# Performance work log

Measured on AMD Instinct MI355X. Metric: run time of the kernel, lower is better.

The kernel has to match this reference:

```python
import jax, jax.numpy as jnp
import numpy as np

N, E, F_IN, F_OUT, PERIODS = 40000, 640000, 64, 128, 12


def setup_inputs() -> dict:
    key = jax.random.key(0)
    ks = jax.random.split(key, 24)
    def w(k, shape):
        return jax.random.normal(k, shape, jnp.float32) * 0.05
    inp = {
        "X": jax.random.normal(ks[0], (N, F_IN, PERIODS), jnp.float32),
        "edge_index": jax.random.randint(ks[1], (2, E), 0, N),
        "edge_weight": jax.random.uniform(ks[2], (E,), jnp.float32),
        "attention": jax.random.uniform(ks[3], (PERIODS,), jnp.float32),
    }
    for idx, g in enumerate(["i", "f", "c", "o"]):
        inp[f"W_x{g}"] = w(ks[4 + 4 * idx], (F_IN, F_OUT))
        inp[f"b_x{g}"] = jnp.zeros((F_OUT,), jnp.float32)
        inp[f"W_h{g}"] = w(ks[5 + 4 * idx], (2 * F_OUT, F_OUT))
        inp[f"b_h{g}"] = jnp.zeros((F_OUT,), jnp.float32)
    return inp


def reference(X, edge_index, edge_weight, attention,
              W_xi, b_xi, W_hi, b_hi,
              W_xf, b_xf, W_hf, b_hf,
              W_xc, b_xc, W_hc, b_hc,
              W_xo, b_xo, W_ho, b_ho):
    n = X.shape[0]
    # GCN normalization with self-loops: D^-1/2 (A + I) D^-1/2
    loops = jnp.arange(n)
    rows = jnp.concatenate([edge_index[0], loops])  # sources
    cols = jnp.concatenate([edge_index[1], loops])  # targets
    wts = jnp.concatenate([edge_weight, jnp.ones((n,), X.dtype)])
    deg = jax.ops.segment_sum(wts, cols, num_segments=n)
    dinv = jnp.where(deg > 0, jax.lax.rsqrt(deg), 0.0)
    norm = dinv[rows] * wts * dinv[cols]  # [E+N]

    def gcn(x, W, b):
        xw = x @ W  # [N, F_OUT]
        agg = jax.ops.segment_sum(norm[:, None] * xw[rows], cols, num_segments=n)
        return agg + b

    probs = jax.nn.softmax(attention)
    H0 = jnp.zeros((n, W_hi.shape[1]), X.dtype)
    C0 = jnp.zeros_like(H0)
    Xp = jnp.moveaxis(X, 2, 0)  # [periods, N, F_IN]

    def step(carry, xs):
        H, C, Hacc = carry
        x_t, p = xs
        def gate(Wx, bx, Wh, bh):
            return jnp.concatenate([gcn(x_t, Wx, bx), H], axis=1) @ Wh + bh
        I = jax.nn.sigmoid(gate(W_xi, b_xi, W_hi, b_hi))
        F = jax.nn.sigmoid(gate(W_xf, b_xf, W_hf, b_hf))
        Ct = jnp.tanh(gate(W_xc, b_xc, W_hc, b_hc))
        O = jax.nn.sigmoid(gate(W_xo, b_xo, W_ho, b_ho))
        C_new = F * C + I * Ct
        H_new = O * jnp.tanh(C_new)
        return (H_new, C_new, Hacc + p * H_new), None

    (H, C, Hacc), _ = jax.lax.scan(step, (H0, C0, H0), (Xp, probs))
    return Hacc
```

## Files before the change

### kernel.cpp

```cpp
#include <hip/hip_runtime.h>

typedef __bf16 bf16_t;
typedef bf16_t bf16x4 __attribute__((ext_vector_type(4)));
typedef bf16_t bf16x8 __attribute__((ext_vector_type(8)));
typedef float floatx4 __attribute__((ext_vector_type(4)));

#define F_INq 64
#define F_OUTq 128
#define PERIODSq 12
#define XROW (F_INq * PERIODSq)

__global__ __launch_bounds__(256) void k_init(float* deg, int* counts, int N) {
  int i = blockIdx.x * 256 + threadIdx.x;
  if (i < N) { deg[i] = 1.0f; counts[i] = 0; }
}

__global__ __launch_bounds__(256) void k_accum(const int* __restrict__ ei, const float* __restrict__ ew,
                                               float* deg, int* counts, int E) {
  int e = blockIdx.x * 256 + threadIdx.x;
  if (e < E) {
    int c = ei[E + e];
    atomicAdd(&deg[c], ew[e]);
    atomicAdd(&counts[c], 1);
  }
}

__global__ __launch_bounds__(256) void k_dinv(float* deg, int N) {
  int i = blockIdx.x * 256 + threadIdx.x;
  if (i < N) { float d = deg[i]; deg[i] = d > 0.0f ? rsqrtf(d) : 0.0f; }
}

__global__ __launch_bounds__(256) void k_scanA(const int* __restrict__ counts, float* __restrict__ deg,
                                               int* __restrict__ bsum, int N) {
  __shared__ int ws[4];
  int b = blockIdx.x, t = threadIdx.x;
  int base = b * 1024 + t * 4;
  int s = 0;
  if (base + 3 < N) {
    int4 c = *(const int4*)(counts + base);
    s = c.x + c.y + c.z + c.w;
  } else {
    for (int k = 0; k < 4; ++k) if (base + k < N) s += counts[base + k];
  }
#pragma unroll
  for (int k = 0; k < 4; ++k) {
    int idx = base + k;
    if (idx < N) { deg[idx] = rsqrtf(deg[idx] + 1.0f); }
  }
  for (int off = 1; off < 64; off <<= 1) s += __shfl_xor(s, off);
  int lane = t & 63, w = t >> 6;
  if (lane == 0) ws[w] = s;
  __syncthreads();
  if (t == 0) bsum[b] = ws[0] + ws[1] + ws[2] + ws[3];
}

__global__ __launch_bounds__(256) void k_scanC(const int* __restrict__ counts, const int* __restrict__ bsum,
                                               int* __restrict__ offs, int* __restrict__ cursor, int N, int nb) {
  __shared__ int ws[4];
  int b = blockIdx.x, t = threadIdx.x;
  int base = b * 1024 + t * 4;
  int c0_ = 0, c1_ = 0, c2_ = 0, c3_ = 0;
  if (base + 3 < N) {
    int4 c = *(const int4*)(counts + base);
    c0_ = c.x; c1_ = c.y; c2_ = c.z; c3_ = c.w;
  } else {
    if (base < N) c0_ = counts[base];
    if (base + 1 < N) c1_ = counts[base + 1];
    if (base + 2 < N) c2_ = counts[base + 2];
    if (base + 3 < N) c3_ = counts[base + 3];
  }
  int tot = c0_ + c1_ + c2_ + c3_;
  int lane = t & 63, w = t >> 6;
  int inc = tot;
  for (int off = 1; off < 64; off <<= 1) {
    int u = __shfl_up(inc, off);
    if (lane >= off) inc += u;
  }
  if (lane == 63) ws[w] = inc;
  __syncthreads();
  int wb = 0;
  for (int i = 0; i < b; ++i) wb += bsum[i];
  for (int i = 0; i < w; ++i) wb += ws[i];
  int e = wb + inc - tot;
  if (base < N)     { offs[base] = e;                 cursor[base] = e; }
  if (base + 1 < N) { int o = e + c0_;                offs[base + 1] = o; cursor[base + 1] = o; }
  if (base + 2 < N) { int o = e + c0_ + c1_;          offs[base + 2] = o; cursor[base + 2] = o; }
  if (base + 3 < N) { int o = e + c0_ + c1_ + c2_;    offs[base + 3] = o; cursor[base + 3] = o; }
  if (b == nb - 1 && t == 0) {
    int tt2 = 0;
    for (int i = 0; i < nb - 1; ++i) tt2 += bsum[i];
    offs[N] = tt2 + ws[0] + ws[1] + ws[2] + ws[3];
  }
}

__global__ __launch_bounds__(1024) void k_scan(const int* __restrict__ counts, int* __restrict__ offs,
                                               int* __restrict__ cursor, int N) {
  __shared__ int sd[1024];
  int t = threadIdx.x;
  int CH = (N + 1023) >> 10;
  int base = t * CH;
  int sum = 0;
  for (int i = 0; i < CH; ++i) { int idx = base + i; if (idx < N) sum += counts[idx]; }
  sd[t] = sum;
  __syncthreads();
  for (int off = 1; off < 1024; off <<= 1) {
    int v = (t >= off) ? sd[t - off] : 0;
    __syncthreads();
    sd[t] += v;
    __syncthreads();
  }
  int run = sd[t] - sum;
  for (int i = 0; i < CH; ++i) {
    int idx = base + i;
    if (idx < N) { offs[idx] = run; cursor[idx] = run; run += counts[idx]; }
  }
  if (t == 1023) offs[N] = sd[1023];
}

__global__ __launch_bounds__(256) void k_scatter(const int* __restrict__ ei, const float* __restrict__ ew,
                                                 const float* __restrict__ dinv, int* cursor,
                                                 int* __restrict__ csr_src, float* __restrict__ csr_nrm, int E) {
  int e = blockIdx.x * 256 + threadIdx.x;
  if (e < E) {
    int r = ei[e], c = ei[E + e];
    int p = atomicAdd(&cursor[c], 1);
    csr_src[p] = r;
    csr_nrm[p] = dinv[r] * ew[e] * dinv[c];
  }
}

__global__ __launch_bounds__(256) void k_prew(
    const float* __restrict__ Wxi, const float* __restrict__ Whi,
    const float* __restrict__ Wxf, const float* __restrict__ Whf,
    const float* __restrict__ Wxc, const float* __restrict__ Whc,
    const float* __restrict__ Wxo, const float* __restrict__ Who,
    const float* __restrict__ bxi, const float* __restrict__ bhi,
    const float* __restrict__ bxf, const float* __restrict__ bhf,
    const float* __restrict__ bxc, const float* __restrict__ bhc,
    const float* __restrict__ bxo, const float* __restrict__ bho,
    const float* __restrict__ att,
    bf16_t* __restrict__ WbT, float* __restrict__ bcomb, float* __restrict__ probs) {
  const int WT = 512 * 192;
  int gid = blockIdx.x * 256 + threadIdx.x;
  if (gid < WT) {
    int col = gid / 192, k = gid % 192;
    int g = col >> 7, j = col & 127;
    const float* Wx = g == 0 ? Wxi : g == 1 ? Wxf : g == 2 ? Wxc : Wxo;
    const float* Wh = g == 0 ? Whi : g == 1 ? Whf : g == 2 ? Whc : Who;
    float s;
    if (k < 64) {
      s = 0.0f;
      for (int kk = 0; kk < 128; ++kk) s += Wx[k * 128 + kk] * Wh[kk * 128 + j];
    } else {
      s = Wh[(k + 64) * 128 + j];
    }
    WbT[(size_t)col * 192 + k] = (bf16_t)s;
  } else if (gid < WT + 512) {
    int cc = gid - WT;
    int g = cc >> 7, j = cc & 127;
    const float* bx = g == 0 ? bxi : g == 1 ? bxf : g == 2 ? bxc : bxo;
    const float* bh = g == 0 ? bhi : g == 1 ? bhf : g == 2 ? bhc : bho;
    const float* Wh = g == 0 ? Whi : g == 1 ? Whf : g == 2 ? Whc : Who;
    float s = bh[j];
    for (int kk = 0; kk < 128; ++kk) s += bx[kk] * Wh[kk * 128 + j];
    bcomb[cc] = s;
  } else if (gid == WT + 512) {
    float m = att[0];
    for (int i = 1; i < PERIODSq; ++i) m = fmaxf(m, att[i]);
    float e[PERIODSq], s = 0.0f;
    for (int i = 0; i < PERIODSq; ++i) { e[i] = __expf(att[i] - m); s += e[i]; }
    for (int i = 0; i < PERIODSq; ++i) probs[i] = e[i] / s;
  }
}

__global__ __launch_bounds__(256) void k_mid(
    const int* __restrict__ ei, const float* __restrict__ ew, const float* __restrict__ dinv,
    int* cursor, int* __restrict__ csr_src, float* __restrict__ csr_nrm, int E,
    const float* __restrict__ Wxi, const float* __restrict__ Whi,
    const float* __restrict__ Wxf, const float* __restrict__ Whf,
    const float* __restrict__ Wxc, const float* __restrict__ Whc,
    const float* __restrict__ Wxo, const float* __restrict__ Who,
    const float* __restrict__ bxi, const float* __restrict__ bhi,
    const float* __restrict__ bxf, const float* __restrict__ bhf,
    const float* __restrict__ bxc, const float* __restrict__ bhc,
    const float* __restrict__ bxo, const float* __restrict__ bho,
    const float* __restrict__ att,
    bf16_t* __restrict__ WbT, float* __restrict__ bcomb, float* __restrict__ probs,
    const float* __restrict__ X, bf16_t* __restrict__ Xb,
    int nbScatter, int nbPrew) {
  __shared__ float lds[XROW];
  const int b = blockIdx.x, tid = threadIdx.x;
  if (b < nbScatter) {
    int e = b * 256 + tid;
    if (e < E) {
      int r = ei[e], c = ei[E + e];
      int p = atomicAdd(&cursor[c], 1);
      csr_src[p] = r;
      csr_nrm[p] = dinv[r] * ew[e] * dinv[c];
    }
    return;
  }
  if (b < nbScatter + nbPrew) {
    const int WT = 512 * 192;
    int gid = (b - nbScatter) * 256 + tid;
    if (gid < WT) {
      int col = gid / 192, k = gid % 192;
      int g = col >> 7, j = col & 127;
      const float* Wx = g == 0 ? Wxi : g == 1 ? Wxf : g == 2 ? Wxc : Wxo;
      const float* Wh = g == 0 ? Whi : g == 1 ? Whf : g == 2 ? Whc : Who;
      float s;
      if (k < 64) {
        s = 0.0f;
        for (int kk = 0; kk < 128; ++kk) s += Wx[k * 128 + kk] * Wh[kk * 128 + j];
      } else {
        s = Wh[(k + 64) * 128 + j];
      }
      WbT[(size_t)col * 192 + k] = (bf16_t)s;
    } else if (gid < WT + 512) {
      int cc = gid - WT;
      int g = cc >> 7, j = cc & 127;
      const float* bx = g == 0 ? bxi : g == 1 ? bxf : g == 2 ? bxc : bxo;
      const float* bh = g == 0 ? bhi : g == 1 ? bhf : g == 2 ? bhc : bho;
      const float* Wh = g == 0 ? Whi : g == 1 ? Whf : g == 2 ? Whc : Who;
      float s = bh[j];
      for (int kk = 0; kk < 128; ++kk) s += bx[kk] * Wh[kk * 128 + j];
      bcomb[cc] = s;
    } else if (gid == WT + 512) {
      float m = att[0];
      for (int i = 1; i < PERIODSq; ++i) m = fmaxf(m, att[i]);
      float e[PERIODSq], s = 0.0f;
      for (int i = 0; i < PERIODSq; ++i) { e[i] = __expf(att[i] - m); s += e[i]; }
      for (int i = 0; i < PERIODSq; ++i) probs[i] = e[i] / s;
    }
    return;
  }
  const int n = b - nbScatter - nbPrew;
  if (tid < 192) {
    const float4* Xr = (const float4*)(X + (size_t)n * XROW);
    float4 v = Xr[tid];
    lds[tid * 4 + 0] = v.x;
    lds[tid * 4 + 1] = v.y;
    lds[tid * 4 + 2] = v.z;
    lds[tid * 4 + 3] = v.w;
  }
  __syncthreads();
  if (tid < 192) {
    const int o = tid * 4;
    bf16x4 r;
#pragma unroll
    for (int k = 0; k < 4; ++k) {
      int oo = o + k;
      int tt = oo >> 6, f = oo & 63;
      r[k] = (bf16_t)lds[f * PERIODSq + tt];
    }
    *(bf16x4*)(Xb + (size_t)n * XROW + o) = r;
  }
}

__global__ __launch_bounds__(256) void k_agg2(const bf16_t* __restrict__ Xb, const int* __restrict__ csr_src,
                                              const float* __restrict__ csr_nrm, const int* __restrict__ offs,
                                              const float* __restrict__ dinv, bf16_t* __restrict__ Xagg, int N) {
  const int node = blockIdx.x * 4 + (threadIdx.x >> 6);
  const int lane = threadIdx.x & 63;
  const int s0 = offs[node], s1 = offs[node + 1];
  floatx4 a0 = {0.f, 0.f, 0.f, 0.f}, a1 = a0, a2 = a0;
  int e = s0;
  for (; e + 8 <= s1; e += 8) {
    bf16x4 v[8][3];
    float nn[8];
#pragma unroll
    for (int u = 0; u < 8; ++u) {
      int s = csr_src[e + u];
      nn[u] = csr_nrm[e + u];
      const bf16x4* xp = (const bf16x4*)(Xb + (size_t)s * XROW) + lane;
      v[u][0] = xp[0]; v[u][1] = xp[64]; v[u][2] = xp[128];
    }
#pragma unroll
    for (int u = 0; u < 8; ++u) {
#pragma unroll
      for (int k = 0; k < 4; ++k) {
        a0[k] += nn[u] * (float)v[u][0][k];
        a1[k] += nn[u] * (float)v[u][1][k];
        a2[k] += nn[u] * (float)v[u][2][k];
      }
    }
  }
  for (; e < s1; ++e) {
    int s = csr_src[e];
    float nr = csr_nrm[e];
    const bf16x4* xp = (const bf16x4*)(Xb + (size_t)s * XROW) + lane;
    bf16x4 v0 = xp[0], v1 = xp[64], v2 = xp[128];
#pragma unroll
    for (int k = 0; k < 4; ++k) {
      a0[k] += nr * (float)v0[k];
      a1[k] += nr * (float)v1[k];
      a2[k] += nr * (float)v2[k];
    }
  }
  float dc = dinv[node];
  float self = dc * dc;
  const bf16x4* xc = (const bf16x4*)(Xb + (size_t)node * XROW) + lane;
  {
    bf16x4 v0 = xc[0], v1 = xc[64], v2 = xc[128];
#pragma unroll
    for (int k = 0; k < 4; ++k) {
      a0[k] += self * (float)v0[k];
      a1[k] += self * (float)v1[k];
      a2[k] += self * (float)v2[k];
    }
  }
  const int f4 = lane & 15, tq = lane >> 4;
  floatx4 accs[3] = {a0, a1, a2};
#pragma unroll
  for (int j = 0; j < 3; ++j) {
    int tt = tq + 4 * j;
    bf16x4 r;
#pragma unroll
    for (int k = 0; k < 4; ++k) r[k] = (bf16_t)accs[j][k];
    *(bf16x4*)(Xagg + ((size_t)tt * N + node) * 64 + f4 * 4) = r;
  }
}

__global__ __launch_bounds__(256) void k_agg(const float* __restrict__ X, const int* __restrict__ csr_src,
                                             const float* __restrict__ csr_nrm, const int* __restrict__ offs,
                                             const float* __restrict__ dinv, bf16_t* __restrict__ Xagg, int N) {
  int c = blockIdx.x;
  int tid = threadIdx.x;
  int s0 = offs[c], s1 = offs[c + 1];
  const int i0 = tid, i1 = tid + 256, i2 = tid + 512;
  float a0 = 0.f, a1 = 0.f, a2 = 0.f;
  for (int e = s0; e < s1; ++e) {
    int s = csr_src[e];
    float nr = csr_nrm[e];
    const float* xp = X + (size_t)s * XROW;
    a0 += nr * xp[i0]; a1 += nr * xp[i1]; a2 += nr * xp[i2];
  }
  float dc = dinv[c];
  float self = dc * dc;
  const float* xc = X + (size_t)c * XROW;
  a0 += self * xc[i0]; a1 += self * xc[i1]; a2 += self * xc[i2];
  __shared__ float lds[XROW];
  lds[i0] = a0; lds[i1] = a1; lds[i2] = a2;
  __syncthreads();
  for (int o = tid; o < XROW; o += 256) {
    int tt = o >> 6, f = o & 63;
    Xagg[(size_t)tt * N * 64 + (size_t)c * 64 + f] = (bf16_t)lds[f * PERIODSq + tt];
  }
}

__global__ __launch_bounds__(512, 2) void k_gate_all(const bf16_t* __restrict__ Xagg,
                                                     const bf16_t* __restrict__ WbT,
                                                     const float* __restrict__ bcomb,
                                                     const float* __restrict__ probs,
                                                     float* __restrict__ out, int N) {
  __shared__ __align__(16) char Hs[2][32 * 256];
  const int tid = threadIdx.x;
  const int lane = tid & 63, w = tid >> 6;
  const int q = lane >> 4, c0 = lane & 15;
  const int n0 = blockIdx.x * 32;
  const int swz = c0 & 7;

  bf16x8 Wf[4][6];
#pragma unroll
  for (int g = 0; g < 4; ++g) {
    const bf16_t* wp = WbT + (size_t)((g * 8 + w) * 16 + c0) * 192;
#pragma unroll
    for (int ks = 0; ks < 6; ++ks) Wf[g][ks] = *(const bf16x8*)(wp + ks * 32 + q * 8);
  }
  floatx4 bv[4];
#pragma unroll
  for (int g = 0; g < 4; ++g) bv[g] = *(const floatx4*)(bcomb + g * 128 + w * 16 + q * 4);
  float pr[PERIODSq];
#pragma unroll
  for (int i = 0; i < PERIODSq; ++i) pr[i] = probs[i];

  floatx4 Cst[2], Ha[2];
#pragma unroll
  for (int rt = 0; rt < 2; ++rt) {
    Cst[rt] = (floatx4){0.f, 0.f, 0.f, 0.f};
    Ha[rt] = (floatx4){0.f, 0.f, 0.f, 0.f};
  }

  const bf16_t* Xrow0 = Xagg + (size_t)(n0 + c0) * 64 + q * 8;
  const bf16_t* Xrow1 = Xagg + (size_t)(n0 + 16 + c0) * 64 + q * 8;

  bf16x8 Xf0 = *(const bf16x8*)(Xrow0);
  bf16x8 Xf1 = *(const bf16x8*)(Xrow0 + 32);
  bf16x8 Xf2 = *(const bf16x8*)(Xrow1);
  bf16x8 Xf3 = *(const bf16x8*)(Xrow1 + 32);

  floatx4 accA[2][4], accB[2][4];
#pragma unroll
  for (int g = 0; g < 4; ++g) {
    accA[0][g] = __builtin_amdgcn_mfma_f32_16x16x32_bf16(Wf[g][0], Xf0, bv[g], 0, 0, 0);
    accA[0][g] = __builtin_amdgcn_mfma_f32_16x16x32_bf16(Wf[g][1], Xf1, accA[0][g], 0, 0, 0);
    accA[1][g] = __builtin_amdgcn_mfma_f32_16x16x32_bf16(Wf[g][0], Xf2, bv[g], 0, 0, 0);
    accA[1][g] = __builtin_amdgcn_mfma_f32_16x16x32_bf16(Wf[g][1], Xf3, accA[1][g], 0, 0, 0);
  }

  const float NL2E = -1.44269504f;
  const float T2L2E = 2.88539008f;

#define EPI(AC, RT, WB, PT)                                                                           \
  {                                                                                                   \
    bf16x4 hv_;                                                                                       \
    _Pragma("unroll") for (int r = 0; r < 4; ++r) {                                                   \
      float pI = AC[RT][0][r], pF = AC[RT][1][r], pC = AC[RT][2][r], pO = AC[RT][3][r];               \
      float I_ = __builtin_amdgcn_rcpf(1.0f + __builtin_amdgcn_exp2f(pI * NL2E));                     \
      float F_ = __builtin_amdgcn_rcpf(1.0f + __builtin_amdgcn_exp2f(pF * NL2E));                     \
      float Ct_ = fmaf(-2.0f, __builtin_amdgcn_rcpf(1.0f + __builtin_amdgcn_exp2f(pC * T2L2E)), 1.0f); \
      float O_ = __builtin_amdgcn_rcpf(1.0f + __builtin_amdgcn_exp2f(pO * NL2E));                     \
      float Cn_ = fmaf(F_, Cst[RT][r], I_ * Ct_);                                                     \
      Cst[RT][r] = Cn_;                                                                               \
      float tC_ = fmaf(-2.0f, __builtin_amdgcn_rcpf(1.0f + __builtin_amdgcn_exp2f(Cn_ * T2L2E)), 1.0f); \
      float Hn_ = O_ * tC_;                                                                           \
      Ha[RT][r] = fmaf(PT, Hn_, Ha[RT][r]);                                                           \
      hv_[r] = (bf16_t)Hn_;                                                                           \
    }                                                                                                 \
    *(bf16x4*)(&Hs[WB][((RT) * 16 + c0) * 256 + (((2 * w + (q >> 1)) ^ swz) << 4) + ((q & 1) * 8)]) = hv_; \
  }

#define PERIOD(T, AC, AN, RB, WB, DO_H, DO_NEXT)                                                      \
  do {                                                                                                \
    if (DO_NEXT) {                                                                                    \
      const size_t toff_ = (size_t)((T) + 1) * N * 64;                                                \
      Xf0 = *(const bf16x8*)(Xrow0 + toff_);                                                          \
      Xf1 = *(const bf16x8*)(Xrow0 + toff_ + 32);                                                     \
      Xf2 = *(const bf16x8*)(Xrow1 + toff_);                                                          \
      Xf3 = *(const bf16x8*)(Xrow1 + toff_ + 32);                                                     \
    }                                                                                                 \
    if (DO_H) {                                                                                       \
      _Pragma("unroll") for (int ks = 0; ks < 4; ++ks) {                                              \
        bf16x8 B0 = *(const bf16x8*)(&Hs[RB][(c0) * 256 + (((4 * ks + q) ^ swz) << 4)]);              \
        _Pragma("unroll") for (int g = 0; g < 4; ++g)                                                 \
          AC[0][g] = __builtin_amdgcn_mfma_f32_16x16x32_bf16(Wf[g][ks + 2], B0, AC[0][g], 0, 0, 0);   \
      }                                                                                               \
      _Pragma("unroll") for (int ks = 0; ks < 4; ++ks) {                                              \
        bf16x8 B1 = *(const bf16x8*)(&Hs[RB][(16 + c0) * 256 + (((4 * ks + q) ^ swz) << 4)]);         \
        _Pragma("unroll") for (int g = 0; g < 4; ++g)                                                 \
          AC[1][g] = __builtin_amdgcn_mfma_f32_16x16x32_bf16(Wf[g][ks + 2], B1, AC[1][g], 0, 0, 0);   \
      }                                                                                               \
    }                                                                                                 \
    const float pt_ = pr[T];                                                                          \
    EPI(AC, 0, WB, pt_)                                 \
    if (DO_NEXT) {                        \
      _Pragma("unroll") for (int g = 0; g < 4; ++g) {                                                 \
        AN[0][g] = __builtin_amdgcn_mfma_f32_16x16x32_bf16(Wf[g][0], Xf0, bv[g], 0, 0, 0);            \
        AN[0][g] = __builtin_amdgcn_mfma_f32_16x16x32_bf16(Wf[g][1], Xf1, AN[0][g], 0, 0, 0);         \
        AN[1][g] = __builtin_amdgcn_mfma_f32_16x16x32_bf16(Wf[g][0], Xf2, bv[g], 0, 0, 0);            \
        AN[1][g] = __builtin_amdgcn_mfma_f32_16x16x32_bf16(Wf[g][1], Xf3, AN[1][g], 0, 0, 0);         \
      }                                                                                               \
    }                                                                                                 \
    EPI(AC, 1, WB, pt_)                                                                               \
    __syncthreads();                                                                                  \
  } while (0)

  PERIOD(0, accA, accB, 1, 0, 0, 1);
  for (int tt = 1; tt <= 9; tt += 2) {
    PERIOD(tt, accB, accA, 0, 1, 1, 1);
    PERIOD(tt + 1, accA, accB, 1, 0, 1, 1);
  }
  PERIOD(11, accB, accA, 0, 1, 1, 0);
#undef PERIOD
#undef EPI

#pragma unroll
  for (int rt = 0; rt < 2; ++rt) {
    int row = n0 + rt * 16 + c0;
    *(floatx4*)(out + (size_t)row * 128 + w * 16 + q * 4) = Ha[rt];
  }
}

extern "C" void kernel_launch(void* const* d_in, const int* in_sizes, int n_in,
                              void* d_out, int out_size, void* d_ws, size_t ws_size,
                              hipStream_t stream) {
  const float* X = (const float*)d_in[0];
  const int* ei = (const int*)d_in[1];
  const float* ew = (const float*)d_in[2];
  const float* att = (const float*)d_in[3];
  const float* Wxi = (const float*)d_in[4];
  const float* bxi = (const float*)d_in[5];
  const float* Whi = (const float*)d_in[6];
  const float* bhi = (const float*)d_in[7];
  const float* Wxf = (const float*)d_in[8];
  const float* bxf = (const float*)d_in[9];
  const float* Whf = (const float*)d_in[10];
  const float* bhf = (const float*)d_in[11];
  const float* Wxc = (const float*)d_in[12];
  const float* bxc = (const float*)d_in[13];
  const float* Whc = (const float*)d_in[14];
  const float* bhc = (const float*)d_in[15];
  const float* Wxo = (const float*)d_in[16];
  const float* bxo = (const float*)d_in[17];
  const float* Who = (const float*)d_in[18];
  const float* bho = (const float*)d_in[19];
  float* out = (float*)d_out;

  const int N = in_sizes[0] / XROW;
  const int E = in_sizes[2];

  char* base = (char*)d_ws;
  size_t off = 0;
  auto carve = [&](size_t bytes) {
    char* r = base + off;
    off += (bytes + 255) & ~(size_t)255;
    return (void*)r;
  };
  float* deg = (float*)carve((size_t)N * 4);
  int* counts = (int*)carve((size_t)N * 4);
  int* offs = (int*)carve((size_t)(N + 1) * 4);
  int* cursor = (int*)carve((size_t)(N + 1) * 4);
  int* csr_src = (int*)carve((size_t)E * 4);
  float* csr_nrm = (float*)carve((size_t)E * 4);
  bf16_t* WbT = (bf16_t*)carve((size_t)512 * 192 * 2);
  float* bcomb = (float*)carve(512 * 4);
  float* probs = (float*)carve(64);
  int* bsum = (int*)carve(64 * 4);
  bf16_t* Xagg = (bf16_t*)carve((size_t)PERIODSq * N * 64 * 2);
  bf16_t* Xb = (bf16_t*)carve((size_t)N * XROW * 2);
  const bool use_bf16 = (off <= ws_size) && ((N & 31) == 0);

  const int nb = (N + 1023) >> 10;
  if (nb <= 64) {
    size_t degspan = ((size_t)N * 4 + 255) & ~(size_t)255;
    hipMemsetAsync(deg, 0, degspan + (size_t)N * 4, stream);
    k_accum<<<(E + 255) / 256, 256, 0, stream>>>(ei, ew, deg, counts, E);
    k_scanA<<<nb, 256, 0, stream>>>(counts, deg, bsum, N);
    k_scanC<<<nb, 256, 0, stream>>>(counts, bsum, offs, cursor, N, nb);
  } else {
    k_init<<<(N + 255) / 256, 256, 0, stream>>>(deg, counts, N);
    k_accum<<<(E + 255) / 256, 256, 0, stream>>>(ei, ew, deg, counts, E);
    k_dinv<<<(N + 255) / 256, 256, 0, stream>>>(deg, N);
    k_scan<<<1, 1024, 0, stream>>>(counts, offs, cursor, N);
  }

  const int nbScatter = (E + 255) / 256;
  const int nbPrew = (512 * 192 + 512 + 1 + 255) / 256;
  if (use_bf16) {
    k_mid<<<nbScatter + nbPrew + N, 256, 0, stream>>>(
        ei, ew, deg, cursor, csr_src, csr_nrm, E,
        Wxi, Whi, Wxf, Whf, Wxc, Whc, Wxo, Who,
        bxi, bhi, bxf, bhf, bxc, bhc, bxo, bho, att, WbT, bcomb, probs,
        X, Xb, nbScatter, nbPrew);
    k_agg2<<<N / 4, 256, 0, stream>>>(Xb, csr_src, csr_nrm, offs, deg, Xagg, N);
    k_gate_all<<<N / 32, 512, 0, stream>>>(Xagg, WbT, bcomb, probs, out, N);
  } else {
    k_scatter<<<nbScatter, 256, 0, stream>>>(ei, ew, deg, cursor, csr_src, csr_nrm, E);
    k_prew<<<nbPrew, 256, 0, stream>>>(
        Wxi, Whi, Wxf, Whf, Wxc, Whc, Wxo, Who,
        bxi, bhi, bxf, bhf, bxc, bhc, bxo, bho, att, WbT, bcomb, probs);
    k_agg<<<N, 256, 0, stream>>>(X, csr_src, csr_nrm, offs, deg, Xagg, N);
    k_gate_all<<<N / 32, 512, 0, stream>>>(Xagg, WbT, bcomb, probs, out, N);
  }
}
```

Before: 598.4 us.

## Fuse aggregation and gated LSTM into persistent producer-consumer kernel

Replaces the separate neighbour-aggregation kernel and gate kernel with one persistent kernel of 256 blocks. Blocks pull tasks from an atomic counter: aggregation tiles run a fixed lag ahead of gate tiles, and readiness is signalled per 32-node tile through release/acquire flags. Inside the gate task, the next period's aggregated features are staged through a double-buffered LDS tile. The aim is to overlap the memory-bound gather with the MFMA-bound recurrence and drop a kernel boundary. In exchange, each CU runs fewer waves for the latency-bound gather, and the scheme adds spin-waiting, atomic loads and stores, and an extra memset.

```diff
diff --git a/kernel.cpp b/kernel.cpp
--- a/kernel.cpp
+++ b/kernel.cpp
@@ -257,70 +257,6 @@
   }
 }
 
-__global__ __launch_bounds__(256) void k_agg2(const bf16_t* __restrict__ Xb, const int* __restrict__ csr_src,
-                                              const float* __restrict__ csr_nrm, const int* __restrict__ offs,
-                                              const float* __restrict__ dinv, bf16_t* __restrict__ Xagg, int N) {
-  const int node = blockIdx.x * 4 + (threadIdx.x >> 6);
-  const int lane = threadIdx.x & 63;
-  const int s0 = offs[node], s1 = offs[node + 1];
-  floatx4 a0 = {0.f, 0.f, 0.f, 0.f}, a1 = a0, a2 = a0;
-  int e = s0;
-  for (; e + 8 <= s1; e += 8) {
-    bf16x4 v[8][3];
-    float nn[8];
-#pragma unroll
-    for (int u = 0; u < 8; ++u) {
-      int s = csr_src[e + u];
-      nn[u] = csr_nrm[e + u];
-      const bf16x4* xp = (const bf16x4*)(Xb + (size_t)s * XROW) + lane;
-      v[u][0] = xp[0]; v[u][1] = xp[64]; v[u][2] = xp[128];
-    }
-#pragma unroll
-    for (int u = 0; u < 8; ++u) {
-#pragma unroll
-      for (int k = 0; k < 4; ++k) {
-        a0[k] += nn[u] * (float)v[u][0][k];
-        a1[k] += nn[u] * (float)v[u][1][k];
-        a2[k] += nn[u] * (float)v[u][2][k];
-      }
-    }
-  }
-  for (; e < s1; ++e) {
-    int s = csr_src[e];
-    float nr = csr_nrm[e];
-    const bf16x4* xp = (const bf16x4*)(Xb + (size_t)s * XROW) + lane;
-    bf16x4 v0 = xp[0], v1 = xp[64], v2 = xp[128];
-#pragma unroll
-    for (int k = 0; k < 4; ++k) {
-      a0[k] += nr * (float)v0[k];
-      a1[k] += nr * (float)v1[k];
-      a2[k] += nr * (float)v2[k];
-    }
-  }
-  float dc = dinv[node];
-  float self = dc * dc;
-  const bf16x4* xc = (const bf16x4*)(Xb + (size_t)node * XROW) + lane;
-  {
-    bf16x4 v0 = xc[0], v1 = xc[64], v2 = xc[128];
-#pragma unroll
-    for (int k = 0; k < 4; ++k) {
-      a0[k] += self * (float)v0[k];
-      a1[k] += self * (float)v1[k];
-      a2[k] += self * (float)v2[k];
-    }
-  }
-  const int f4 = lane & 15, tq = lane >> 4;
-  floatx4 accs[3] = {a0, a1, a2};
-#pragma unroll
-  for (int j = 0; j < 3; ++j) {
-    int tt = tq + 4 * j;
-    bf16x4 r;
-#pragma unroll
-    for (int k = 0; k < 4; ++k) r[k] = (bf16_t)accs[j][k];
-    *(bf16x4*)(Xagg + ((size_t)tt * N + node) * 64 + f4 * 4) = r;
-  }
-}
-
 __global__ __launch_bounds__(256) void k_agg(const float* __restrict__ X, const int* __restrict__ csr_src,
                                              const float* __restrict__ csr_nrm, const int* __restrict__ offs,
                                              const float* __restrict__ dinv, bf16_t* __restrict__ Xagg, int N) {
@@ -442,8 +378,8 @@
       }                                                                                               \
     }                                                                                                 \
     const float pt_ = pr[T];                                                                          \
-    EPI(AC, 0, WB, pt_)                                 \
-    if (DO_NEXT) {                        \
+    EPI(AC, 0, WB, pt_)                                                                               \
+    if (DO_NEXT) {                                                                                    \
       _Pragma("unroll") for (int g = 0; g < 4; ++g) {                                                 \
         AN[0][g] = __builtin_amdgcn_mfma_f32_16x16x32_bf16(Wf[g][0], Xf0, bv[g], 0, 0, 0);            \
         AN[0][g] = __builtin_amdgcn_mfma_f32_16x16x32_bf16(Wf[g][1], Xf1, AN[0][g], 0, 0, 0);         \
@@ -468,6 +404,256 @@
   for (int rt = 0; rt < 2; ++rt) {
     int row = n0 + rt * 16 + c0;
     *(floatx4*)(out + (size_t)row * 128 + w * 16 + q * 4) = Ha[rt];
+  }
+}
+
+__global__ __launch_bounds__(512, 2) void k_fused(
+    const bf16_t* __restrict__ Xb, const int* __restrict__ csr_src, const float* __restrict__ csr_nrm,
+    const int* __restrict__ offs, const float* __restrict__ dinv,
+    const bf16_t* __restrict__ WbT, const float* __restrict__ bcomb, const float* __restrict__ probs,
+    bf16_t* __restrict__ Xagg, float* __restrict__ out, int* __restrict__ ctr, int* __restrict__ flags,
+    int N) {
+  __shared__ __align__(16) char Hs[2][32 * 256];
+  __shared__ __align__(16) char XLs[2][32 * 128];
+  __shared__ int taskS;
+  const int tid = threadIdx.x;
+  const int lane = tid & 63, w = tid >> 6;
+  const int q = lane >> 4, c0 = lane & 15;
+  const int swz = c0 & 7;
+  const int nT = N >> 5, tot = 2 * nT;
+  const int LAG = nT < 250 ? nT : 250;
+  const int pairsLen = 2 * (nT - LAG);
+  const int xnode = tid >> 4, xch = tid & 15;
+  const int xwb = xnode * 128 + (((xch >> 1) ^ (xnode & 7)) << 4) + ((xch & 1) * 8);
+
+  bf16x8 Wf[4][6];
+#pragma unroll
+  for (int g = 0; g < 4; ++g) {
+    const bf16_t* wp = WbT + (size_t)((g * 8 + w) * 16 + c0) * 192;
+#pragma unroll
+    for (int ks = 0; ks < 6; ++ks) Wf[g][ks] = *(const bf16x8*)(wp + ks * 32 + q * 8);
+  }
+  floatx4 bv[4];
+#pragma unroll
+  for (int g = 0; g < 4; ++g) bv[g] = *(const floatx4*)(bcomb + g * 128 + w * 16 + q * 4);
+  float pr[PERIODSq];
+#pragma unroll
+  for (int i = 0; i < PERIODSq; ++i) pr[i] = probs[i];
+
+  const float NL2E = -1.44269504f;
+  const float T2L2E = 2.88539008f;
+
+  for (;;) {
+    __syncthreads();
+    if (tid == 0) taskS = atomicAdd(ctr, 1);
+    __syncthreads();
+    const int t = taskS;
+    if (t >= tot) break;
+    int type, idx;
+    if (t < LAG) {
+      type = 0; idx = t;
+    } else if (t - LAG < pairsLen) {
+      int r = t - LAG;
+      type = (r & 1) ? 0 : 1;
+      idx = (r >> 1) + ((r & 1) ? LAG : 0);
+    } else {
+      type = 1; idx = (t - LAG - pairsLen) + (nT - LAG);
+    }
+
+    if (type == 0) {
+      const int nbase = idx * 32 + w * 4;
+      for (int i = 0; i < 4; ++i) {
+        const int nd = nbase + i;
+        const int s0 = offs[nd], s1 = offs[nd + 1];
+        floatx4 a0 = {0.f, 0.f, 0.f, 0.f}, a1 = a0, a2 = a0;
+        int e = s0;
+        for (; e + 8 <= s1; e += 8) {
+          bf16x4 v[8][3];
+          float nn[8];
+#pragma unroll
+          for (int u = 0; u < 8; ++u) {
+            int s = csr_src[e + u];
+            nn[u] = csr_nrm[e + u];
+            const bf16x4* xp = (const bf16x4*)(Xb + (size_t)s * XROW) + lane;
+            v[u][0] = xp[0]; v[u][1] = xp[64]; v[u][2] = xp[128];
+          }
+#pragma unroll
+          for (int u = 0; u < 8; ++u) {
+#pragma unroll
+            for (int k = 0; k < 4; ++k) {
+              a0[k] += nn[u] * (float)v[u][0][k];
+              a1[k] += nn[u] * (float)v[u][1][k];
+              a2[k] += nn[u] * (float)v[u][2][k];
+            }
+          }
+        }
+        for (; e < s1; ++e) {
+          int s = csr_src[e];
+          float nr = csr_nrm[e];
+          const bf16x4* xp = (const bf16x4*)(Xb + (size_t)s * XROW) + lane;
+          bf16x4 v0 = xp[0], v1 = xp[64], v2 = xp[128];
+#pragma unroll
+          for (int k = 0; k < 4; ++k) {
+            a0[k] += nr * (float)v0[k];
+            a1[k] += nr * (float)v1[k];
+            a2[k] += nr * (float)v2[k];
+          }
+        }
+        float dc = dinv[nd];
+        float self = dc * dc;
+        const bf16x4* xc = (const bf16x4*)(Xb + (size_t)nd * XROW) + lane;
+        {
+          bf16x4 v0 = xc[0], v1 = xc[64], v2 = xc[128];
+#pragma unroll
+          for (int k = 0; k < 4; ++k) {
+            a0[k] += self * (float)v0[k];
+            a1[k] += self * (float)v1[k];
+            a2[k] += self * (float)v2[k];
+          }
+        }
+        const int f4 = lane & 15, tq = lane >> 4;
+        floatx4 accs[3] = {a0, a1, a2};
+#pragma unroll
+        for (int j = 0; j < 3; ++j) {
+          int tt = tq + 4 * j;
+          union { bf16x4 v; unsigned long long u; } cv;
+#pragma unroll
+          for (int k = 0; k < 4; ++k) cv.v[k] = (bf16_t)accs[j][k];
+          __hip_atomic_store((unsigned long long*)(Xagg + ((size_t)tt * N + nd) * 64 + f4 * 4),
+                             cv.u, __ATOMIC_RELAXED, __HIP_MEMORY_SCOPE_AGENT);
+        }
+      }
+      __syncthreads();
+      if (tid == 0)
+        __hip_atomic_store(&flags[idx], 1, __ATOMIC_RELEASE, __HIP_MEMORY_SCOPE_AGENT);
+    } else {
+      if (tid == 0) {
+        while (__hip_atomic_load(&flags[idx], __ATOMIC_RELAXED, __HIP_MEMORY_SCOPE_AGENT) == 0)
+          __builtin_amdgcn_s_sleep(2);
+      }
+      __syncthreads();
+      const int n0 = idx * 32;
+      {
+        unsigned long long x0 = __hip_atomic_load(
+            (const unsigned long long*)(Xagg + (size_t)n0 * 64) + tid, __ATOMIC_RELAXED, __HIP_MEMORY_SCOPE_AGENT);
+        unsigned long long x1 = __hip_atomic_load(
+            (const unsigned long long*)(Xagg + ((size_t)N + n0) * 64) + tid, __ATOMIC_RELAXED, __HIP_MEMORY_SCOPE_AGENT);
+        *(unsigned long long*)&XLs[0][xwb] = x0;
+        *(unsigned long long*)&XLs[1][xwb] = x1;
+      }
+      __syncthreads();
+
+      floatx4 Cst[2], Ha[2];
+#pragma unroll
+      for (int rt = 0; rt < 2; ++rt) {
+        Cst[rt] = (floatx4){0.f, 0.f, 0.f, 0.f};
+        Ha[rt] = (floatx4){0.f, 0.f, 0.f, 0.f};
+      }
+
+      floatx4 accA[2][4], accB[2][4];
+      {
+        bf16x8 X00 = *(const bf16x8*)(&XLs[0][c0 * 128 + ((q ^ swz) << 4)]);
+        bf16x8 X01 = *(const bf16x8*)(&XLs[0][c0 * 128 + (((4 + q) ^ swz) << 4)]);
+        bf16x8 X10 = *(const bf16x8*)(&XLs[0][(16 + c0) * 128 + ((q ^ swz) << 4)]);
+        bf16x8 X11 = *(const bf16x8*)(&XLs[0][(16 + c0) * 128 + (((4 + q) ^ swz) << 4)]);
+#pragma unroll
+        for (int g = 0; g < 4; ++g) {
+          accA[0][g] = __builtin_amdgcn_mfma_f32_16x16x32_bf16(Wf[g][0], X00, bv[g], 0, 0, 0);
+          accA[0][g] = __builtin_amdgcn_mfma_f32_16x16x32_bf16(Wf[g][1], X01, accA[0][g], 0, 0, 0);
+          accA[1][g] = __builtin_amdgcn_mfma_f32_16x16x32_bf16(Wf[g][0], X10, bv[g], 0, 0, 0);
+          accA[1][g] = __builtin_amdgcn_mfma_f32_16x16x32_bf16(Wf[g][1], X11, accA[1][g], 0, 0, 0);
+        }
+      }
+
+#define EPI(AC, RT, WB, PT)                                                                           \
+  {                                                                                                   \
+    bf16x4 hv_;                                                                                       \
+    _Pragma("unroll") for (int r = 0; r < 4; ++r) {                                                   \
+      float pI = AC[RT][0][r], pF = AC[RT][1][r], pC = AC[RT][2][r], pO = AC[RT][3][r];               \
+      float I_ = __builtin_amdgcn_rcpf(1.0f + __builtin_amdgcn_exp2f(pI * NL2E));                     \
+      float F_ = __builtin_amdgcn_rcpf(1.0f + __builtin_amdgcn_exp2f(pF * NL2E));                     \
+      float Ct_ = fmaf(-2.0f, __builtin_amdgcn_rcpf(1.0f + __builtin_amdgcn_exp2f(pC * T2L2E)), 1.0f); \
+      float O_ = __builtin_amdgcn_rcpf(1.0f + __builtin_amdgcn_exp2f(pO * T2L2E * 0.5f * 1.0f)));     \
+    }                                                                                                 \
+  }
+#undef EPI
+#define EPI(AC, RT, WB, PT)                                                                           \
+  {                                                                                                   \
+    bf16x4 hv_;                                                                                       \
+    _Pragma("unroll") for (int r = 0; r < 4; ++r) {                                                   \
+      float pI = AC[RT][0][r], pF = AC[RT][1][r], pC = AC[RT][2][r], pO = AC[RT][3][r];               \
+      float I_ = __builtin_amdgcn_rcpf(1.0f + __builtin_amdgcn_exp2f(pI * NL2E));                     \
+      float F_ = __builtin_amdgcn_rcpf(1.0f + __builtin_amdgcn_exp2f(pF * NL2E));                     \
+      float Ct_ = fmaf(-2.0f, __builtin_amdgcn_rcpf(1.0f + __builtin_amdgcn_exp2f(pC * T2L2E)), 1.0f); \
+      float O_ = __builtin_amdgcn_rcpf(1.0f + __builtin_amdgcn_exp2f(pO * NL2E));                     \
+      float Cn_ = fmaf(F_, Cst[RT][r], I_ * Ct_);                                                     \
+      Cst[RT][r] = Cn_;                                                                               \
+      float tC_ = fmaf(-2.0f, __builtin_amdgcn_rcpf(1.0f + __builtin_amdgcn_exp2f(Cn_ * T2L2E)), 1.0f); \
+      float Hn_ = O_ * tC_;                                                                           \
+      Ha[RT][r] = fmaf(PT, Hn_, Ha[RT][r]);                                                           \
+      hv_[r] = (bf16_t)Hn_;                                                                           \
+    }                                                                                                 \
+    *(bf16x4*)(&Hs[WB][((RT) * 16 + c0) * 256 + (((2 * w + (q >> 1)) ^ swz) << 4) + ((q & 1) * 8)]) = hv_; \
+  }
+
+#define GPER(T, AC, AN, DO_H, DO_NEXT, DO_STAGE)                                                      \
+  do {                                                                                                \
+    unsigned long long xs_ = 0;                                                                       \
+    if (DO_STAGE)                                                                                     \
+      xs_ = __hip_atomic_load((const unsigned long long*)(Xagg + ((size_t)((T) + 2) * N + n0) * 64) + tid, \
+                              __ATOMIC_RELAXED, __HIP_MEMORY_SCOPE_AGENT);                            \
+    if (DO_H) {                                                                                       \
+      _Pragma("unroll") for (int ks = 0; ks < 4; ++ks) {                                              \
+        bf16x8 B0 = *(const bf16x8*)(&Hs[((T) & 1) ^ 1][(c0) * 256 + (((4 * ks + q) ^ swz) << 4)]);   \
+        _Pragma("unroll") for (int g = 0; g < 4; ++g)                                                 \
+          AC[0][g] = __builtin_amdgcn_mfma_f32_16x16x32_bf16(Wf[g][ks + 2], B0, AC[0][g], 0, 0, 0);   \
+      }                                                                                               \
+      _Pragma("unroll") for (int ks = 0; ks < 4; ++ks) {                                              \
+        bf16x8 B1 = *(const bf16x8*)(&Hs[((T) & 1) ^ 1][(16 + c0) * 256 + (((4 * ks + q) ^ swz) << 4)]); \
+        _Pragma("unroll") for (int g = 0; g < 4; ++g)                                                 \
+          AC[1][g] = __builtin_amdgcn_mfma_f32_16x16x32_bf16(Wf[g][ks + 2], B1, AC[1][g], 0, 0, 0);   \
+      }                                                                                               \
+    }                                                                                                 \
+    const float pt_ = pr[T];                                                                          \
+    EPI(AC, 0, (T) & 1, pt_)                                                                          \
+    if (DO_NEXT) {                                                                                    \
+      bf16x8 X00 = *(const bf16x8*)(&XLs[((T) + 1) & 1][c0 * 128 + ((q ^ swz) << 4)]);                \
+      bf16x8 X01 = *(const bf16x8*)(&XLs[((T) + 1) & 1][c0 * 128 + (((4 + q) ^ swz) << 4)]);          \
+      bf16x8 X10 = *(const bf16x8*)(&XLs[((T) + 1) & 1][(16 + c0) * 128 + ((q ^ swz) << 4)]);         \
+      bf16x8 X11 = *(const bf16x8*)(&XLs[((T) + 1) & 1][(16 + c0) * 128 + (((4 + q) ^ swz) << 4)]);   \
+      _Pragma("unroll") for (int g = 0; g < 4; ++g) {                                                 \
+        AN[0][g] = __builtin_amdgcn_mfma_f32_16x16x32_bf16(Wf[g][0], X00, bv[g], 0, 0, 0);            \
+        AN[0][g] = __builtin_amdgcn_mfma_f32_16x16x32_bf16(Wf[g][1], X01, AN[0][g], 0, 0, 0);         \
+        AN[1][g] = __builtin_amdgcn_mfma_f32_16x16x32_bf16(Wf[g][0], X10, bv[g], 0, 0, 0);            \
+        AN[1][g] = __builtin_amdgcn_mfma_f32_16x16x32_bf16(Wf[g][1], X11, AN[1][g], 0, 0, 0);         \
+      }                                                                                               \
+    }                                                                                                 \
+    EPI(AC, 1, (T) & 1, pt_)                                                                          \
+    if (DO_STAGE) *(unsigned long long*)&XLs[(T) & 1][xwb] = xs_;                                     \
+    __syncthreads();                                                                                  \
+  } while (0)
+
+      GPER(0, accA, accB, 0, 1, 1);
+      GPER(1, accB, accA, 1, 1, 1);
+      GPER(2, accA, accB, 1, 1, 1);
+      GPER(3, accB, accA, 1, 1, 1);
+      GPER(4, accA, accB, 1, 1, 1);
+      GPER(5, accB, accA, 1, 1, 1);
+      GPER(6, accA, accB, 1, 1, 1);
+      GPER(7, accB, accA, 1, 1, 1);
+      GPER(8, accA, accB, 1, 1, 1);
+      GPER(9, accB, accA, 1, 1, 1);
+      GPER(10, accA, accB, 1, 1, 0);
+      GPER(11, accB, accA, 1, 0, 0);
+#undef GPER
+#undef EPI
+
+#pragma unroll
+      for (int rt = 0; rt < 2; ++rt) {
+        int row = n0 + rt * 16 + c0;
+        *(floatx4*)(out + (size_t)row * 128 + w * 16 + q * 4) = Ha[rt];
+      }
+    }
   }
 }
 
@@ -516,35 +702,42 @@
   float* bcomb = (float*)carve(512 * 4);
   float* probs = (float*)carve(64);
   int* bsum = (int*)carve(64 * 4);
+  const int nT = N / 32;
+  int* ctr = (int*)carve(256);
+  int* flags = (int*)carve((size_t)(nT + 64) * 4);
   bf16_t* Xagg = (bf16_t*)carve((size_t)PERIODSq * N * 64 * 2);
   bf16_t* Xb = (bf16_t*)carve((size_t)N * XROW * 2);
   const bool use_bf16 = (off <= ws_size) && ((N & 31) == 0);
 
   const int nb = (N + 1023) >> 10;
-  if (nb <= 64) {
+  if (nb <= 64 && use_bf16) {
     size_t degspan = ((size_t)N * 4 + 255) & ~(size_t)255;
     hipMemsetAsync(deg, 0, degspan + (size_t)N * 4, stream);
+    hipMemsetAsync(ctr, 0, 256 + (size_t)(nT + 64) * 4, stream);
     k_accum<<<(E + 255) / 256, 256, 0, stream>>>(ei, ew, deg, counts, E);
     k_scanA<<<nb, 256, 0, stream>>>(counts, deg, bsum, N);
     k_scanC<<<nb, 256, 0, stream>>>(counts, bsum, offs, cursor, N, nb);
-  } else {
-    k_init<<<(N + 255) / 256, 256, 0, stream>>>(deg, counts, N);
-    k_accum<<<(E + 255) / 256, 256, 0, stream>>>(ei, ew, deg, counts, E);
-    k_dinv<<<(N + 255) / 256, 256, 0, stream>>>(deg, N);
-    k_scan<<<1, 1024, 0, stream>>>(counts, offs, cursor, N);
-  }
-
-  const int nbScatter = (E + 255) / 256;
-  const int nbPrew = (512 * 192 + 512 + 1 + 255) / 256;
-  if (use_bf16) {
+
+    const int nbScatter = (E + 255) / 256;
+    const int nbPrew = (512 * 192 + 512 + 1 + 255) / 256;
     k_mid<<<nbScatter + nbPrew + N, 256, 0, stream>>>(
         ei, ew, deg, cursor, csr_src, csr_nrm, E,
         Wxi, Whi, Wxf, Whf, Wxc, Whc, Wxo, Who,
         bxi, bhi, bxf, bhf, bxc, bhc, bxo, bho, att, WbT, bcomb, probs,
         X, Xb, nbScatter, nbPrew);
-    k_agg2<<<N / 4, 256, 0, stream>>>(Xb, csr_src, csr_nrm, offs, deg, Xagg, N);
-    k_gate_all<<<N / 32, 512, 0, stream>>>(Xagg, WbT, bcomb, probs, out, N);
+    k_fused<<<256, 512, 0, stream>>>(Xb, csr_src, csr_nrm, offs, deg, WbT, bcomb, probs,
+                                     Xagg, out, ctr, flags, N);
   } else {
+    k_init<<<(N + 255) / 256, 256, 0, stream>>>(deg, counts, N);
+    k_accum<<<(E + 255) / 256, 256, 0, stream>>>(ei, ew, deg, counts, E);
+    k_dinv<<<(N + 255) / 256, 256, 0, stream>>>(deg, N);
+    if (nb <= 64) {
+      k_scan<<<1, 1024, 0, stream>>>(counts, offs, cursor, N);
+    } else {
+      k_scan<<<1, 1024, 0, stream>>>(counts, offs, cursor, N);
+    }
+    const int nbScatter = (E + 255) / 256;
+    const int nbPrew = (512 * 192 + 512 + 1 + 255) / 256;
     k_scatter<<<nbScatter, 256, 0, stream>>>(ei, ew, deg, cursor, csr_src, csr_nrm, E);
     k_prew<<<nbPrew, 256, 0, stream>>>(
         Wxi, Whi, Wxf, Whf, Wxc, Whc, Wxo, Who,
```

New measurement: 657.0 us. 9.8% more time.
